# Kernel optimization log

Measured on AMD Instinct MI355X. Metric: run time of the kernel, lower is better.

The kernel has to match this reference:

```python
import jax, jax.numpy as jnp
import numpy as np

WH, WW = 8, 8            # window_size
N_TOK = WH * WW          # tokens per window = 64
DIM = 128
HEADS = 4
HEAD_DIM = DIM // HEADS  # 32
B_WIN = 4096             # batch * num_windows
EPS = 1e-6


def _swin_relative_index():
    # standard Swin relative_position_index, shape (N, N), values in [0, (2Wh-1)*(2Ww-1))
    coords = np.stack(np.meshgrid(np.arange(WH), np.arange(WW), indexing='ij'))  # (2, Wh, Ww)
    coords = coords.reshape(2, -1)                                               # (2, N)
    rel = coords[:, :, None] - coords[:, None, :]                                # (2, N, N)
    rel = rel.transpose(1, 2, 0).astype(np.int32)                                # (N, N, 2)
    rel[..., 0] += WH - 1
    rel[..., 1] += WW - 1
    rel[..., 0] *= 2 * WW - 1
    return rel.sum(-1)                                                           # (N, N)


def _coords_grid():
    # normalized relative coordinate table, shape ((2Wh-1)*(2Ww-1), 2) in [-1, 1]
    rh = np.arange(-(WH - 1), WH, dtype=np.float32) / max(WH - 1, 1)
    rw = np.arange(-(WW - 1), WW, dtype=np.float32) / max(WW - 1, 1)
    return np.stack(np.meshgrid(rh, rw, indexing='ij'), -1).reshape(-1, 2)


def setup_inputs() -> dict:
    key = jax.random.key(0)
    ks = jax.random.split(key, 8)
    s = 0.02
    return {
        'x':       jax.random.normal(ks[0], (B_WIN, N_TOK, DIM), jnp.float32),
        'W_qkv':   jax.random.normal(ks[1], (DIM, 3 * DIM), jnp.float32) * s,
        'W_proj':  jax.random.normal(ks[2], (DIM, DIM), jnp.float32) * s,
        'b_proj':  jnp.zeros((DIM,), jnp.float32),
        'cpb_w1':  jax.random.normal(ks[3], (2, 512), jnp.float32) * s,
        'cpb_b1':  jnp.zeros((512,), jnp.float32),
        'cpb_w2':  jax.random.normal(ks[4], (512, HEADS), jnp.float32) * s,
        'h_times':   jnp.float32(2.0),
        'pow_para':  jnp.float32(0.0),
        'ws_scalar': jnp.float32(1.0),
        'ws_scalar2': jnp.float32(2.0),
        'rel_index': jnp.asarray(_swin_relative_index()),          # (N, N) int32
        'coords':    jnp.asarray(_coords_grid()),                  # (225, 2) float32
    }


def reference(x, W_qkv, W_proj, b_proj, cpb_w1, cpb_b1, cpb_w2,
              h_times, pow_para, ws_scalar, ws_scalar2, rel_index, coords):
    B, N, C = x.shape
    scale = HEAD_DIM ** -0.5

    # qkv projection (bias=False), split into heads
    qkv = (x @ W_qkv).reshape(B, N, 3, HEADS, HEAD_DIM)
    qkv = jnp.transpose(qkv, (2, 0, 3, 1, 4))           # (3, B, H, N, hd)
    q, k, v = qkv[0], qkv[1], qkv[2]

    attn = jnp.einsum('bhnd,bhmd->bhnm', q, k) * scale  # (B, H, N, N)

    # dynamic position bias: parametrized coord transform -> small MLP -> gather
    ht = jax.nn.softplus(h_times)
    pp = jax.nn.sigmoid(pow_para)
    ws = jax.nn.softplus(ws_scalar) / jax.nn.softplus(ws_scalar2)
    t = coords * ht                                      # (225, 2)
    t = jnp.sign(t) * (jnp.abs(t) + EPS) ** pp * ws      # pow_mode coord warp
    bias_table = jax.nn.relu(t @ cpb_w1 + cpb_b1) @ cpb_w2   # (225, H)
    bias = bias_table[rel_index]                         # (N, N, H)
    attn = attn + jnp.transpose(bias, (2, 0, 1))[None]   # (B, H, N, N)

    attn = jax.nn.softmax(attn, axis=-1)
    out = jnp.einsum('bhnm,bhmd->bnhd', attn, v).reshape(B, N, C)
    return out @ W_proj + b_proj
```

## Files before the change

kernel.cpp:

```cpp
#include <hip/hip_runtime.h>
#include <hip/hip_bf16.h>

typedef __hip_bfloat16 bf16;
typedef __bf16 bf8v __attribute__((ext_vector_type(8)));
typedef float f4v __attribute__((ext_vector_type(4)));

#define WS_BIAS   0
#define WS_TABLE  32768
#define WS_QKVT   36864
#define WS_PROJT  135168
#define WS_FLAG   167936

__device__ __forceinline__ float rdf(const void* p, int i, int isbf) {
  return isbf ? __bfloat162float(((const bf16*)p)[i]) : ((const float*)p)[i];
}

__global__ void detect_dtype(const unsigned short* __restrict__ coords_raw,
                             char* __restrict__ ws) {
  *(int*)(ws + WS_FLAG) = (coords_raw[0] != 0) ? 1 : 0;
}

__global__ void prep_transpose(const void* __restrict__ Wqkv,
                               const void* __restrict__ Wproj,
                               char* __restrict__ ws) {
  int idx = blockIdx.x * 256 + threadIdx.x;
  int isbf = *(const int*)(ws + WS_FLAG);
  bf16* qt = (bf16*)(ws + WS_QKVT);
  bf16* pt = (bf16*)(ws + WS_PROJT);
  if (idx < 384 * 128) {
    int c = idx >> 7, k = idx & 127;
    qt[idx] = __float2bfloat16(rdf(Wqkv, k * 384 + c, isbf));
  } else {
    int j = idx - 384 * 128;
    int c = j >> 7, k = j & 127;
    pt[j] = __float2bfloat16(rdf(Wproj, k * 128 + c, isbf));
  }
}

__global__ void prep_table(const void* __restrict__ coords,
                           const void* __restrict__ w1,
                           const void* __restrict__ b1,
                           const void* __restrict__ w2,
                           const void* __restrict__ hts,
                           const void* __restrict__ pps,
                           const void* __restrict__ ws1,
                           const void* __restrict__ ws2,
                           char* __restrict__ ws) {
  __shared__ float red[8][4];
  const int r = blockIdx.x;
  const int j = threadIdx.x;
  const int isbf = *(const int*)(ws + WS_FLAG);
  float* table = (float*)(ws + WS_TABLE);

  float ht  = log1pf(__expf(rdf(hts, 0, isbf)));
  float pp  = 1.f / (1.f + __expf(-rdf(pps, 0, isbf)));
  float wsv = log1pf(__expf(rdf(ws1, 0, isbf))) /
              log1pf(__expf(rdf(ws2, 0, isbf)));
  float t0 = rdf(coords, 2 * r + 0, isbf) * ht;
  float t1 = rdf(coords, 2 * r + 1, isbf) * ht;
  float s0 = (t0 > 0.f) ? 1.f : ((t0 < 0.f) ? -1.f : 0.f);
  float s1 = (t1 > 0.f) ? 1.f : ((t1 < 0.f) ? -1.f : 0.f);
  float u0 = s0 * __powf(fabsf(t0) + 1e-6f, pp) * wsv;
  float u1 = s1 * __powf(fabsf(t1) + 1e-6f, pp) * wsv;

  float h = u0 * rdf(w1, j, isbf) + u1 * rdf(w1, 512 + j, isbf) + rdf(b1, j, isbf);
  h = fmaxf(h, 0.f);
  float a[4];
#pragma unroll
  for (int q = 0; q < 4; ++q) a[q] = h * rdf(w2, 4 * j + q, isbf);
#pragma unroll
  for (int off = 1; off < 64; off <<= 1)
#pragma unroll
    for (int q = 0; q < 4; ++q) a[q] += __shfl_xor(a[q], off);
  int wv = j >> 6, ln = j & 63;
  if (ln == 0) {
#pragma unroll
    for (int q = 0; q < 4; ++q) red[wv][q] = a[q];
  }
  __syncthreads();
  if (j < 4) {
    float s = 0.f;
#pragma unroll
    for (int w8 = 0; w8 < 8; ++w8) s += red[w8][j];
    table[r * 4 + j] = s;
  }
}

__global__ void prep_gather(const int* __restrict__ rel, char* __restrict__ ws) {
  int pos = blockIdx.x * 256 + threadIdx.x;
  const float* table = (const float*)(ws + WS_TABLE);
  bf16* bias = (bf16*)(ws + WS_BIAS);
  int h = pos >> 10, rest = pos & 1023;
  int mt = rest >> 8, n4 = (rest >> 6) & 3, quad = (rest >> 4) & 3, l16 = rest & 15;
  int jj = n4 * 16 + l16;
  union { uint2 u; bf16 hh[4]; } pk;
#pragma unroll
  for (int r = 0; r < 4; ++r) {
    int i = mt * 16 + quad * 4 + r;
    int rr = rel[i * 64 + jj];
    pk.hh[r] = __float2bfloat16(table[rr * 4 + h]);
  }
  *(uint2*)(bias + pos * 4) = pk.u;
}

__global__ __launch_bounds__(256, 3) void wattn_main(
    const void* __restrict__ xp,
    const char* __restrict__ ws,
    const void* __restrict__ bprojp,
    void* __restrict__ outp) {
  __shared__ alignas(16) char smem[54272];
  bf16* xls = (bf16*)smem;
  bf16* os  = (bf16*)smem;
  const int tid  = threadIdx.x;
  const int w    = tid >> 6;
  const int lane = tid & 63;
  const int l16  = lane & 15;
  const int quad = lane >> 4;
  bf16* scr = (bf16*)(smem + 17408 + w * 9216);

  const int isbf = *(const int*)(ws + WS_FLAG);
  const bf16* WqkvT  = (const bf16*)(ws + WS_QKVT);
  const bf16* WprojT = (const bf16*)(ws + WS_PROJT);
  const bf16* biasg  = (const bf16*)(ws + WS_BIAS);

  const int b = blockIdx.x;

  if (isbf) {
    const bf16* xb = (const bf16*)xp + (size_t)b * 8192;
#pragma unroll
    for (int it = 0; it < 4; ++it) {
      int e = (tid + it * 256) * 8;
      int row = e >> 7, col = e & 127;
      *(uint4*)(xls + row * 136 + col) = *(const uint4*)(xb + e);
    }
  } else {
    const float* xb = (const float*)xp + (size_t)b * 8192;
#pragma unroll
    for (int it = 0; it < 4; ++it) {
      int e = (tid + it * 256) * 8;
      int row = e >> 7, col = e & 127;
      f4v a = *(const f4v*)(xb + e);
      f4v c = *(const f4v*)(xb + e + 4);
      union { uint4 u; bf16 h[8]; } pk;
#pragma unroll
      for (int jj = 0; jj < 4; ++jj) {
        pk.h[jj]     = __float2bfloat16(a[jj]);
        pk.h[4 + jj] = __float2bfloat16(c[jj]);
      }
      *(uint4*)(xls + row * 136 + col) = pk.u;
    }
  }
  __syncthreads();

  const f4v zf = {0.f, 0.f, 0.f, 0.f};
  bf8v vf[2][2], qf[4], kf[4];

  auto run_qkv = [&](int colbase, f4v (&acc)[4][2]) {
    const bf16* Bb = WqkvT + (size_t)colbase * 128;
#pragma unroll
    for (int ks = 0; ks < 4; ++ks) {
      bf8v xk[4];
#pragma unroll
      for (int mt = 0; mt < 4; ++mt)
        xk[mt] = *(const bf8v*)(xls + (mt * 16 + l16) * 136 + ks * 32 + quad * 8);
#pragma unroll
      for (int nt = 0; nt < 2; ++nt) {
        bf8v bfr = *(const bf8v*)(Bb + (nt * 16 + l16) * 128 + ks * 32 + quad * 8);
#pragma unroll
        for (int mt = 0; mt < 4; ++mt)
          acc[mt][nt] = __builtin_amdgcn_mfma_f32_16x16x32_bf16(xk[mt], bfr, acc[mt][nt], 0, 0, 0);
      }
    }
  };

  {
    f4v acc[4][2];
#pragma unroll
    for (int mt = 0; mt < 4; ++mt) { acc[mt][0] = zf; acc[mt][1] = zf; }
    run_qkv(256 + w * 32, acc);
#pragma unroll
    for (int mt = 0; mt < 4; ++mt)
#pragma unroll
      for (int nt = 0; nt < 2; ++nt) {
        union { uint2 u; bf16 h[4]; } pk;
#pragma unroll
        for (int r = 0; r < 4; ++r) pk.h[r] = __float2bfloat16(acc[mt][nt][r]);
        *(uint2*)(scr + (nt * 16 + l16) * 72 + mt * 16 + quad * 4) = pk.u;
      }
#pragma unroll
    for (int k2 = 0; k2 < 2; ++k2)
#pragma unroll
      for (int nt = 0; nt < 2; ++nt)
        vf[k2][nt] = *(const bf8v*)(scr + (nt * 16 + l16) * 72 + k2 * 32 + quad * 8);
  }

  {
    f4v acc[4][2];
#pragma unroll
    for (int mt = 0; mt < 4; ++mt) { acc[mt][0] = zf; acc[mt][1] = zf; }
    run_qkv(w * 32, acc);
#pragma unroll
    for (int mt = 0; mt < 4; ++mt)
#pragma unroll
      for (int nt = 0; nt < 2; ++nt)
#pragma unroll
        for (int r = 0; r < 4; ++r)
          scr[(mt * 16 + quad * 4 + r) * 40 + nt * 16 + l16] = __float2bfloat16(acc[mt][nt][r]);
#pragma unroll
    for (int mt = 0; mt < 4; ++mt)
      qf[mt] = *(const bf8v*)(scr + (mt * 16 + l16) * 40 + quad * 8);
  }

  {
    f4v acc[4][2];
#pragma unroll
    for (int mt = 0; mt < 4; ++mt) { acc[mt][0] = zf; acc[mt][1] = zf; }
    run_qkv(128 + w * 32, acc);
#pragma unroll
    for (int mt = 0; mt < 4; ++mt)
#pragma unroll
      for (int nt = 0; nt < 2; ++nt)
#pragma unroll
        for (int r = 0; r < 4; ++r)
          scr[(mt * 16 + quad * 4 + r) * 40 + nt * 16 + l16] = __float2bfloat16(acc[mt][nt][r]);
#pragma unroll
    for (int n4 = 0; n4 < 4; ++n4)
      kf[n4] = *(const bf8v*)(scr + (n4 * 16 + l16) * 40 + quad * 8);
  }

  __syncthreads();

  const float scale = 0.1767766952966369f;
  const bf16* bh = biasg + w * 4096;
  for (int mt = 0; mt < 4; ++mt) {
    f4v sc[4];
#pragma unroll
    for (int n4 = 0; n4 < 4; ++n4)
      sc[n4] = __builtin_amdgcn_mfma_f32_16x16x32_bf16(qf[mt], kf[n4], zf, 0, 0, 0);
    float p[4][4];
#pragma unroll
    for (int n4 = 0; n4 < 4; ++n4) {
      union { uint2 u; bf16 hh[4]; } bb;
      bb.u = *(const uint2*)(bh + mt * 1024 + n4 * 256 + quad * 64 + l16 * 4);
#pragma unroll
      for (int r = 0; r < 4; ++r)
        p[n4][r] = sc[n4][r] * scale + __bfloat162float(bb.hh[r]);
    }
#pragma unroll
    for (int r = 0; r < 4; ++r) {
      float m = fmaxf(fmaxf(p[0][r], p[1][r]), fmaxf(p[2][r], p[3][r]));
      m = fmaxf(m, __shfl_xor(m, 1, 16));
      m = fmaxf(m, __shfl_xor(m, 2, 16));
      m = fmaxf(m, __shfl_xor(m, 4, 16));
      m = fmaxf(m, __shfl_xor(m, 8, 16));
      float s = 0.f;
#pragma unroll
      for (int n4 = 0; n4 < 4; ++n4) { p[n4][r] = __expf(p[n4][r] - m); s += p[n4][r]; }
      s += __shfl_xor(s, 1, 16);
      s += __shfl_xor(s, 2, 16);
      s += __shfl_xor(s, 4, 16);
      s += __shfl_xor(s, 8, 16);
      float inv = __builtin_amdgcn_rcpf(s);
#pragma unroll
      for (int n4 = 0; n4 < 4; ++n4) p[n4][r] *= inv;
    }
#pragma unroll
    for (int n4 = 0; n4 < 4; ++n4)
#pragma unroll
      for (int r = 0; r < 4; ++r)
        scr[(mt * 16 + quad * 4 + r) * 72 + n4 * 16 + l16] = __float2bfloat16(p[n4][r]);

    f4v o2[2] = {zf, zf};
#pragma unroll
    for (int k2 = 0; k2 < 2; ++k2) {
      bf8v pf = *(const bf8v*)(scr + (mt * 16 + l16) * 72 + k2 * 32 + quad * 8);
#pragma unroll
      for (int nt = 0; nt < 2; ++nt)
        o2[nt] = __builtin_amdgcn_mfma_f32_16x16x32_bf16(pf, vf[k2][nt], o2[nt], 0, 0, 0);
    }
#pragma unroll
    for (int nt = 0; nt < 2; ++nt) {
      union { uint2 u; bf16 h[4]; } pk;
#pragma unroll
      for (int r = 0; r < 4; ++r) pk.h[r] = __float2bfloat16(o2[nt][r]);
#pragma unroll
      for (int r = 0; r < 4; ++r)
        os[(mt * 16 + quad * 4 + r) * 136 + w * 32 + nt * 16 + l16] = pk.h[r];
    }
  }

  __syncthreads();

  f4v pa[4][2];
#pragma unroll
  for (int mt = 0; mt < 4; ++mt) { pa[mt][0] = zf; pa[mt][1] = zf; }
#pragma unroll
  for (int ks = 0; ks < 4; ++ks) {
    bf8v oa[4];
#pragma unroll
    for (int mt = 0; mt < 4; ++mt)
      oa[mt] = *(const bf8v*)(os + (mt * 16 + l16) * 136 + ks * 32 + quad * 8);
#pragma unroll
    for (int nt = 0; nt < 2; ++nt) {
      bf8v bfr = *(const bf8v*)(WprojT + (size_t)(w * 32 + nt * 16 + l16) * 128 + ks * 32 + quad * 8);
#pragma unroll
      for (int mt = 0; mt < 4; ++mt)
        pa[mt][nt] = __builtin_amdgcn_mfma_f32_16x16x32_bf16(oa[mt], bfr, pa[mt][nt], 0, 0, 0);
    }
  }

  float* fsf = (float*)(smem + 17408);
#pragma unroll
  for (int nt = 0; nt < 2; ++nt) {
    int c = w * 32 + nt * 16 + l16;
    float bb = rdf(bprojp, c, isbf);
#pragma unroll
    for (int mt = 0; mt < 4; ++mt)
#pragma unroll
      for (int r = 0; r < 4; ++r)
        fsf[(mt * 16 + quad * 4 + r) * 128 + c] = pa[mt][nt][r] + bb;
  }
  __syncthreads();

  if (isbf) {
    bf16* ob = (bf16*)outp + (size_t)b * 8192;
#pragma unroll
    for (int it = 0; it < 4; ++it) {
      int e = (tid + it * 256) * 8;
      f4v a = *(const f4v*)(fsf + e);
      f4v c = *(const f4v*)(fsf + e + 4);
      union { uint4 u; bf16 h[8]; } pk;
#pragma unroll
      for (int jj = 0; jj < 4; ++jj) {
        pk.h[jj]     = __float2bfloat16(a[jj]);
        pk.h[4 + jj] = __float2bfloat16(c[jj]);
      }
      *(uint4*)(ob + e) = pk.u;
    }
  } else {
    float* ob = (float*)outp + (size_t)b * 8192;
#pragma unroll
    for (int it = 0; it < 8; ++it) {
      int e = (tid + it * 256) * 4;
      *(f4v*)(ob + e) = *(const f4v*)(fsf + e);
    }
  }
}

extern "C" void kernel_launch(void* const* d_in, const int* in_sizes, int n_in,
                              void* d_out, int out_size, void* d_ws, size_t ws_size,
                              hipStream_t stream) {
  const void* x      = d_in[0];
  const void* Wqkv   = d_in[1];
  const void* Wproj  = d_in[2];
  const void* bproj  = d_in[3];
  const void* w1     = d_in[4];
  const void* b1     = d_in[5];
  const void* w2     = d_in[6];
  const void* hts    = d_in[7];
  const void* pps    = d_in[8];
  const void* ws1    = d_in[9];
  const void* ws2    = d_in[10];
  const int*  rel    = (const int*)d_in[11];
  const void* coords = d_in[12];
  char* ws  = (char*)d_ws;

  detect_dtype<<<1, 1, 0, stream>>>((const unsigned short*)coords, ws);
  prep_transpose<<<256, 256, 0, stream>>>(Wqkv, Wproj, ws);
  prep_table<<<225, 512, 0, stream>>>(coords, w1, b1, w2, hts, pps, ws1, ws2, ws);
  prep_gather<<<16, 256, 0, stream>>>(rel, ws);
  wattn_main<<<4096, 256, 0, stream>>>(x, ws, bproj, d_out);
}
```

Measured before the change: 347.3 us.

## Shrink per-wave LDS scratch and drop fp32 staging to raise occupancy

Reduces the per-wave scratch buffer to one 16-row tile by restructuring the Q/K/V transposes and the P tile round trip so each 16-row tile is written and read back before the next. The fp32 output staging buffer is removed: fp32 outputs are written directly from MFMA registers to global memory, and bf16 outputs are staged in the reused x buffer. This cuts LDS per block from about 53KB to 26KB, and launch bounds are raised to allow 6 blocks per CU. The risks are uncoalesced scalar fp32 global stores, more serialized LDS round trips, and register pressure under the tighter occupancy target.

```diff
diff --git a/kernel.cpp b/kernel.cpp
--- a/kernel.cpp
+++ b/kernel.cpp
@@ -103,12 +103,12 @@
   *(uint2*)(bias + pos * 4) = pk.u;
 }
 
-__global__ __launch_bounds__(256, 3) void wattn_main(
+__global__ __launch_bounds__(256, 6) void wattn_main(
     const void* __restrict__ xp,
     const char* __restrict__ ws,
     const void* __restrict__ bprojp,
     void* __restrict__ outp) {
-  __shared__ alignas(16) char smem[54272];
+  __shared__ alignas(16) char smem[26624];
   bf16* xls = (bf16*)smem;
   bf16* os  = (bf16*)smem;
   const int tid  = threadIdx.x;
@@ -116,7 +116,7 @@
   const int lane = tid & 63;
   const int l16  = lane & 15;
   const int quad = lane >> 4;
-  bf16* scr = (bf16*)(smem + 17408 + w * 9216);
+  bf16* scr = (bf16*)(smem + 17408 + w * 2304);
 
   const int isbf = *(const int*)(ws + WS_FLAG);
   const bf16* WqkvT  = (const bf16*)(ws + WS_QKVT);
@@ -179,19 +179,18 @@
     for (int mt = 0; mt < 4; ++mt) { acc[mt][0] = zf; acc[mt][1] = zf; }
     run_qkv(256 + w * 32, acc);
 #pragma unroll
-    for (int mt = 0; mt < 4; ++mt)
-#pragma unroll
-      for (int nt = 0; nt < 2; ++nt) {
+    for (int nt = 0; nt < 2; ++nt) {
+#pragma unroll
+      for (int mt = 0; mt < 4; ++mt) {
         union { uint2 u; bf16 h[4]; } pk;
 #pragma unroll
         for (int r = 0; r < 4; ++r) pk.h[r] = __float2bfloat16(acc[mt][nt][r]);
-        *(uint2*)(scr + (nt * 16 + l16) * 72 + mt * 16 + quad * 4) = pk.u;
+        *(uint2*)(scr + l16 * 72 + mt * 16 + quad * 4) = pk.u;
       }
 #pragma unroll
-    for (int k2 = 0; k2 < 2; ++k2)
-#pragma unroll
-      for (int nt = 0; nt < 2; ++nt)
-        vf[k2][nt] = *(const bf8v*)(scr + (nt * 16 + l16) * 72 + k2 * 32 + quad * 8);
+      for (int k2 = 0; k2 < 2; ++k2)
+        vf[k2][nt] = *(const bf8v*)(scr + l16 * 72 + k2 * 32 + quad * 8);
+    }
   }
 
   {
@@ -200,15 +199,14 @@
     for (int mt = 0; mt < 4; ++mt) { acc[mt][0] = zf; acc[mt][1] = zf; }
     run_qkv(w * 32, acc);
 #pragma unroll
-    for (int mt = 0; mt < 4; ++mt)
+    for (int mt = 0; mt < 4; ++mt) {
 #pragma unroll
       for (int nt = 0; nt < 2; ++nt)
 #pragma unroll
         for (int r = 0; r < 4; ++r)
-          scr[(mt * 16 + quad * 4 + r) * 40 + nt * 16 + l16] = __float2bfloat16(acc[mt][nt][r]);
-#pragma unroll
-    for (int mt = 0; mt < 4; ++mt)
-      qf[mt] = *(const bf8v*)(scr + (mt * 16 + l16) * 40 + quad * 8);
+          scr[(quad * 4 + r) * 40 + nt * 16 + l16] = __float2bfloat16(acc[mt][nt][r]);
+      qf[mt] = *(const bf8v*)(scr + l16 * 40 + quad * 8);
+    }
   }
 
   {
@@ -217,15 +215,14 @@
     for (int mt = 0; mt < 4; ++mt) { acc[mt][0] = zf; acc[mt][1] = zf; }
     run_qkv(128 + w * 32, acc);
 #pragma unroll
-    for (int mt = 0; mt < 4; ++mt)
+    for (int mt = 0; mt < 4; ++mt) {
 #pragma unroll
       for (int nt = 0; nt < 2; ++nt)
 #pragma unroll
         for (int r = 0; r < 4; ++r)
-          scr[(mt * 16 + quad * 4 + r) * 40 + nt * 16 + l16] = __float2bfloat16(acc[mt][nt][r]);
-#pragma unroll
-    for (int n4 = 0; n4 < 4; ++n4)
-      kf[n4] = *(const bf8v*)(scr + (n4 * 16 + l16) * 40 + quad * 8);
+          scr[(quad * 4 + r) * 40 + nt * 16 + l16] = __float2bfloat16(acc[mt][nt][r]);
+      kf[mt] = *(const bf8v*)(scr + l16 * 40 + quad * 8);
+    }
   }
 
   __syncthreads();
@@ -268,12 +265,12 @@
     for (int n4 = 0; n4 < 4; ++n4)
 #pragma unroll
       for (int r = 0; r < 4; ++r)
-        scr[(mt * 16 + quad * 4 + r) * 72 + n4 * 16 + l16] = __float2bfloat16(p[n4][r]);
+        scr[(quad * 4 + r) * 72 + n4 * 16 + l16] = __float2bfloat16(p[n4][r]);
 
     f4v o2[2] = {zf, zf};
 #pragma unroll
     for (int k2 = 0; k2 < 2; ++k2) {
-      bf8v pf = *(const bf8v*)(scr + (mt * 16 + l16) * 72 + k2 * 32 + quad * 8);
+      bf8v pf = *(const bf8v*)(scr + l16 * 72 + k2 * 32 + quad * 8);
 #pragma unroll
       for (int nt = 0; nt < 2; ++nt)
         o2[nt] = __builtin_amdgcn_mfma_f32_16x16x32_bf16(pf, vf[k2][nt], o2[nt], 0, 0, 0);
@@ -309,40 +306,37 @@
     }
   }
 
-  float* fsf = (float*)(smem + 17408);
-#pragma unroll
-  for (int nt = 0; nt < 2; ++nt) {
-    int c = w * 32 + nt * 16 + l16;
-    float bb = rdf(bprojp, c, isbf);
-#pragma unroll
-    for (int mt = 0; mt < 4; ++mt)
-#pragma unroll
-      for (int r = 0; r < 4; ++r)
-        fsf[(mt * 16 + quad * 4 + r) * 128 + c] = pa[mt][nt][r] + bb;
-  }
-  __syncthreads();
-
-  if (isbf) {
+  if (!isbf) {
+    float* ob = (float*)outp + (size_t)b * 8192;
+#pragma unroll
+    for (int nt = 0; nt < 2; ++nt) {
+      int c = w * 32 + nt * 16 + l16;
+      float bb = ((const float*)bprojp)[c];
+#pragma unroll
+      for (int mt = 0; mt < 4; ++mt)
+#pragma unroll
+        for (int r = 0; r < 4; ++r)
+          ob[(mt * 16 + quad * 4 + r) * 128 + c] = pa[mt][nt][r] + bb;
+    }
+  } else {
+    __syncthreads();
+#pragma unroll
+    for (int nt = 0; nt < 2; ++nt) {
+      int c = w * 32 + nt * 16 + l16;
+      float bb = __bfloat162float(((const bf16*)bprojp)[c]);
+#pragma unroll
+      for (int mt = 0; mt < 4; ++mt)
+#pragma unroll
+        for (int r = 0; r < 4; ++r)
+          xls[(mt * 16 + quad * 4 + r) * 136 + c] = __float2bfloat16(pa[mt][nt][r] + bb);
+    }
+    __syncthreads();
     bf16* ob = (bf16*)outp + (size_t)b * 8192;
 #pragma unroll
     for (int it = 0; it < 4; ++it) {
       int e = (tid + it * 256) * 8;
-      f4v a = *(const f4v*)(fsf + e);
-      f4v c = *(const f4v*)(fsf + e + 4);
-      union { uint4 u; bf16 h[8]; } pk;
-#pragma unroll
-      for (int jj = 0; jj < 4; ++jj) {
-        pk.h[jj]     = __float2bfloat16(a[jj]);
-        pk.h[4 + jj] = __float2bfloat16(c[jj]);
-      }
-      *(uint4*)(ob + e) = pk.u;
-    }
-  } else {
-    float* ob = (float*)outp + (size_t)b * 8192;
-#pragma unroll
-    for (int it = 0; it < 8; ++it) {
-      int e = (tid + it * 256) * 4;
-      *(f4v*)(ob + e) = *(const f4v*)(fsf + e);
+      int row = e >> 7, col = e & 127;
+      *(uint4*)(ob + e) = *(const uint4*)(xls + row * 136 + col);
     }
   }
 }
```

Result: slower. 360.9 us (+3.9%).
